# Optimization experiments

Measured on AMD Instinct MI355X. Metric: run time of the kernel, lower is better.

## Reference

```python
import jax, jax.numpy as jnp
import numpy as np

B, S, D, H = 2, 2048, 1024, 16
DK = D // H
NEG = -1.0e9


def setup_inputs() -> dict:
    key = jax.random.key(0)
    ks = jax.random.split(key, 12)
    scale = 1.0 / np.sqrt(D)
    return {
        "Q": jax.random.normal(ks[0], (B, S, D), jnp.float32),
        "K": jax.random.normal(ks[1], (B, S, D), jnp.float32),
        "V": jax.random.normal(ks[2], (B, S, D), jnp.float32),
        "Wq": jax.random.normal(ks[3], (D, D), jnp.float32) * scale,
        "bq": jnp.zeros((D,), jnp.float32),
        "Wk": jax.random.normal(ks[4], (D, D), jnp.float32) * scale,
        "bk": jnp.zeros((D,), jnp.float32),
        "Wv": jax.random.normal(ks[5], (D, D), jnp.float32) * scale,
        "bv": jnp.zeros((D,), jnp.float32),
        "Wo": jax.random.normal(ks[6], (D, D), jnp.float32) * scale,
        "bo": jnp.zeros((D,), jnp.float32),
        "src_mask": jnp.ones((B, S), jnp.int32),
    }


def reference(Q, K, V, Wq, bq, Wk, bk, Wv, bv, Wo, bo, src_mask):
    # Dropout layers are identity in eval mode.
    def heads(x, W, b):
        y = x @ W + b                      # [B,S,D]
        return y.reshape(B, S, H, DK).transpose(0, 2, 1, 3)  # [B,H,S,DK]

    q = heads(Q, Wq, bq)
    k = heads(K, Wk, bk)
    v = heads(V, Wv, bv)

    scores = jnp.einsum("bhqd,bhkd->bhqk", q, k) / np.sqrt(DK)  # [B,H,S,S]
    mask = src_mask[:, None, None, :]  # [B,1,1,S] broadcasts over heads/queries
    scores = jnp.where(mask == 0, NEG, scores)
    attn = jax.nn.softmax(scores, axis=-1)
    out = jnp.einsum("bhqk,bhkd->bhqd", attn, v)  # [B,H,S,DK]
    out = out.transpose(0, 2, 1, 3).reshape(B, S, D)
    return out @ Wo + bo
```

## Files before the change

kernel.cpp:

```cpp
#include <hip/hip_runtime.h>
#include <hip/hip_bf16.h>
#include <cstdint>

#define B_ 2
#define S_ 2048
#define D_ 1024
#define H_ 16
#define DK_ 64

typedef __bf16 bf16x8 __attribute__((ext_vector_type(8)));
typedef float f32x4 __attribute__((ext_vector_type(4)));
typedef unsigned int u32x4 __attribute__((ext_vector_type(4)));

typedef __attribute__((address_space(3))) void lds_void_t;
typedef const __attribute__((address_space(1))) void gbl_void_t;

__device__ __forceinline__ unsigned short f2bf(float x) {
    unsigned int u = __builtin_bit_cast(unsigned int, x);
    u += 0x7fffu + ((u >> 16) & 1u);
    return (unsigned short)(u >> 16);
}

__device__ __forceinline__ float exp2fast(float x) {
    float r;
    asm("v_exp_f32 %0, %1" : "=v"(r) : "v"(x));
    return r;
}

__device__ __forceinline__ unsigned cvtpk(float a, float b) {
    unsigned r;
    asm("v_cvt_pk_bf16_f32 %0, %1, %2" : "=v"(r) : "v"(a), "v"(b));
    return r;
}

__device__ __forceinline__ void gload16(const void* g, void* lds) {
    __builtin_amdgcn_global_load_lds((gbl_void_t*)(uintptr_t)g,
                                     (lds_void_t*)(unsigned)(uintptr_t)lds,
                                     16, 0, 0);
}

__device__ __forceinline__ bf16x8 lds_read8(const unsigned short* p) {
    return __builtin_bit_cast(bf16x8, *(const u32x4*)p);
}

__device__ __forceinline__ f32x4 mfma16(bf16x8 a, bf16x8 b, f32x4 c) {
    return __builtin_amdgcn_mfma_f32_16x16x32_bf16(a, b, c, 0, 0, 0);
}

__global__ void cast3_kernel(const float* __restrict__ Q, const float* __restrict__ K,
                             const float* __restrict__ V, unsigned short* __restrict__ Qc,
                             unsigned short* __restrict__ Kc, unsigned short* __restrict__ Vc,
                             int n4) {
    const int z = blockIdx.z;
    const float* in = (z == 0) ? Q : (z == 1) ? K : V;
    unsigned short* out = (z == 0) ? Qc : (z == 1) ? Kc : Vc;
    int i = blockIdx.x * 256 + threadIdx.x;
    if (i >= n4) return;
    const float4 v = reinterpret_cast<const float4*>(in)[i];
    unsigned long long pk = (unsigned long long)f2bf(v.x)
                          | ((unsigned long long)f2bf(v.y) << 16)
                          | ((unsigned long long)f2bf(v.z) << 32)
                          | ((unsigned long long)f2bf(v.w) << 48);
    reinterpret_cast<unsigned long long*>(out)[i] = pk;
}

__global__ void transpose4_kernel(const float* __restrict__ Wq, const float* __restrict__ Wk,
                                  const float* __restrict__ Wv, const float* __restrict__ Wo,
                                  unsigned short* __restrict__ WqT, unsigned short* __restrict__ WkT,
                                  unsigned short* __restrict__ WvT, unsigned short* __restrict__ WoT) {
    const int z = blockIdx.z;
    const float* W = (z == 0) ? Wq : (z == 1) ? Wk : (z == 2) ? Wv : Wo;
    unsigned short* Wt = (z == 0) ? WqT : (z == 1) ? WkT : (z == 2) ? WvT : WoT;
    __shared__ float t[32][33];
    const int bx = blockIdx.x, by = blockIdx.y;
    const int tx = threadIdx.x & 31, ty = threadIdx.x >> 5;
#pragma unroll
    for (int j = 0; j < 4; j++)
        t[ty + 8 * j][tx] = W[(size_t)(by * 32 + ty + 8 * j) * D_ + bx * 32 + tx];
    __syncthreads();
#pragma unroll
    for (int j = 0; j < 4; j++)
        Wt[(size_t)(bx * 32 + ty + 8 * j) * D_ + by * 32 + tx] = f2bf(t[tx][ty + 8 * j]);
}

__global__ __launch_bounds__(256, 3) void qkv_gemm(
    const unsigned short* __restrict__ Qc, const unsigned short* __restrict__ Kc,
    const unsigned short* __restrict__ Vc, const unsigned short* __restrict__ WqT,
    const unsigned short* __restrict__ WkT, const unsigned short* __restrict__ WvT,
    const float* __restrict__ bq, const float* __restrict__ bk,
    const float* __restrict__ bvv, unsigned short* __restrict__ qb,
    unsigned short* __restrict__ kb, unsigned short* __restrict__ vTb, float qs) {
    constexpr int Kd = 1024;
    __shared__ __align__(16) unsigned short As[128 * 32];
    __shared__ __align__(16) unsigned short Bs[128 * 32];
    __shared__ __align__(16) unsigned short Cs[128 * 136];
    const int z = blockIdx.z;
    const unsigned short* A  = (z == 0) ? Qc : (z == 1) ? Kc : Vc;
    const unsigned short* Bt = (z == 0) ? WqT : (z == 1) ? WkT : WvT;
    const float* bias = (z == 0) ? bq : (z == 1) ? bk : bvv;
    const float cscale = (z == 0) ? qs : 1.0f;

    const int tid = threadIdx.x;
    const int l = tid & 63, w = tid >> 6;
    const int lr = l & 15, g = l >> 4;
    const int wr = w & 1, wc = w >> 1;
    const int m0 = blockIdx.y * 128, n0 = blockIdx.x * 128;

    f32x4 acc[4][4] = {};

    const int mr = tid >> 2;
    const int kk = (tid & 3) * 8;
    const unsigned short* a_src = A + (size_t)(m0 + mr) * Kd + kk;
    const unsigned short* b_src = Bt + (size_t)(n0 + mr) * Kd + kk;
    char* asb = (char*)As + w * 1024;
    char* bsb = (char*)Bs + w * 1024;

    for (int k0 = 0; k0 < Kd; k0 += 32) {
        __syncthreads();
        gload16(a_src + k0,           asb);
        gload16(a_src + 64 * Kd + k0, asb + 4096);
        gload16(b_src + k0,           bsb);
        gload16(b_src + 64 * Kd + k0, bsb + 4096);
        __syncthreads();
        bf16x8 av[4], bv[4];
#pragma unroll
        for (int mi = 0; mi < 4; mi++)
            av[mi] = lds_read8(&As[(wr * 64 + mi * 16 + lr) * 32 + g * 8]);
#pragma unroll
        for (int ni = 0; ni < 4; ni++)
            bv[ni] = lds_read8(&Bs[(wc * 64 + ni * 16 + lr) * 32 + g * 8]);
#pragma unroll
        for (int mi = 0; mi < 4; mi++)
#pragma unroll
            for (int ni = 0; ni < 4; ni++)
                acc[mi][ni] = mfma16(av[mi], bv[ni], acc[mi][ni]);
    }

    if (z == 2) {
#pragma unroll
        for (int ni = 0; ni < 4; ni++) {
            const int cl = wc * 64 + ni * 16 + lr;
            const float bcol = bias[n0 + cl];
#pragma unroll
            for (int mi = 0; mi < 4; mi++) {
                const int rw = wr * 64 + mi * 16 + 4 * g;
                uint2 pk;
                pk.x = cvtpk(acc[mi][ni][0] + bcol, acc[mi][ni][1] + bcol);
                pk.y = cvtpk(acc[mi][ni][2] + bcol, acc[mi][ni][3] + bcol);
                *reinterpret_cast<uint2*>(&Cs[cl * 136 + rw]) = pk;
            }
        }
        __syncthreads();
        const int s0g = m0 & 2047;
        const int bb  = m0 >> 11;
#pragma unroll
        for (int it = 0; it < 8; ++it) {
            const int cl = it * 16 + (tid >> 4);
            const int sc = tid & 15;
            const int cg = n0 + cl;
            const int hh = cg >> 6, dk = cg & 63;
            const u32x4 vv = *reinterpret_cast<const u32x4*>(&Cs[cl * 136 + sc * 8]);
            *reinterpret_cast<u32x4*>(
                &vTb[(((size_t)(bb * H_ + hh) * DK_ + dk) << 11) + s0g + sc * 8]) = vv;
        }
    } else {
#pragma unroll
        for (int ni = 0; ni < 4; ni++) {
            const int col = n0 + wc * 64 + ni * 16 + lr;
            const float bcol = bias[col];
#pragma unroll
            for (int mi = 0; mi < 4; mi++) {
#pragma unroll
                for (int r = 0; r < 4; r++) {
                    const int row = m0 + wr * 64 + mi * 16 + 4 * g + r;
                    const float v = (acc[mi][ni][r] + bcol) * cscale;
                    const int b = row >> 11, s = row & 2047, h = col >> 6, dk = col & 63;
                    unsigned short* out = z ? kb : qb;
                    out[(((size_t)(b * H_ + h) * S_ + s) << 6) + dk] = f2bf(v);
                }
            }
        }
    }
}

__global__ __launch_bounds__(256, 2) void gemm_out(
    const unsigned short* __restrict__ A, const unsigned short* __restrict__ Bt,
    const float* __restrict__ bias, float* __restrict__ C) {
    constexpr int Kd = 1024;
    __shared__ __align__(16) unsigned short As[128 * 32];
    __shared__ __align__(16) unsigned short Bs[128 * 32];
    const int tid = threadIdx.x;
    const int l = tid & 63, w = tid >> 6;
    const int lr = l & 15, g = l >> 4;
    const int wr = w & 1, wc = w >> 1;
    const int m0 = blockIdx.y * 128, n0 = blockIdx.x * 128;

    f32x4 acc[4][4] = {};
    const int mr = tid >> 2;
    const int kk = (tid & 3) * 8;
    const unsigned short* a_src = A + (size_t)(m0 + mr) * Kd + kk;
    const unsigned short* b_src = Bt + (size_t)(n0 + mr) * Kd + kk;
    char* asb = (char*)As + w * 1024;
    char* bsb = (char*)Bs + w * 1024;

    for (int k0 = 0; k0 < Kd; k0 += 32) {
        __syncthreads();
        gload16(a_src + k0,           asb);
        gload16(a_src + 64 * Kd + k0, asb + 4096);
        gload16(b_src + k0,           bsb);
        gload16(b_src + 64 * Kd + k0, bsb + 4096);
        __syncthreads();
        bf16x8 av[4], bv[4];
#pragma unroll
        for (int mi = 0; mi < 4; mi++)
            av[mi] = lds_read8(&As[(wr * 64 + mi * 16 + lr) * 32 + g * 8]);
#pragma unroll
        for (int ni = 0; ni < 4; ni++)
            bv[ni] = lds_read8(&Bs[(wc * 64 + ni * 16 + lr) * 32 + g * 8]);
#pragma unroll
        for (int mi = 0; mi < 4; mi++)
#pragma unroll
            for (int ni = 0; ni < 4; ni++)
                acc[mi][ni] = mfma16(av[mi], bv[ni], acc[mi][ni]);
    }

#pragma unroll
    for (int ni = 0; ni < 4; ni++) {
        const int col = n0 + wc * 64 + ni * 16 + lr;
        const float bcol = bias[col];
#pragma unroll
        for (int mi = 0; mi < 4; mi++)
#pragma unroll
            for (int r = 0; r < 4; r++) {
                const int row = m0 + wr * 64 + mi * 16 + 4 * g + r;
                C[(size_t)row * D_ + col] = acc[mi][ni][r] + bcol;
            }
    }
}

__global__ __launch_bounds__(512, 4) void attn64(
    const unsigned short* __restrict__ q, const unsigned short* __restrict__ kmat,
    const unsigned short* __restrict__ vT, const int* __restrict__ mask,
    unsigned short* __restrict__ aout) {
    __shared__ __align__(16) unsigned short k_lds[2][64 * 64];
    __shared__ __align__(16) unsigned short v_lds[2][64 * 64];
    __shared__ __align__(16) unsigned short p_lds[8][16 * 72];
    __shared__ int mflag;

    const int tid = threadIdx.x;
    const int l = tid & 63, w = tid >> 6;
    const int lr = l & 15, g = l >> 4;
    const int bh = blockIdx.y;
    const int b = bh >> 4, h = bh & 15;
    const int q0 = blockIdx.x * 128;

    const size_t base = (size_t)bh * S_ * DK_;
    const size_t vbase = (size_t)bh * DK_ * S_;
    const float FM = 14.0f;

    bf16x8 qf[2];
#pragma unroll
    for (int ks = 0; ks < 2; ks++)
        qf[ks] = __builtin_bit_cast(bf16x8,
            *(const u32x4*)(q + base + (size_t)(q0 + w * 16 + lr) * 64 + ks * 32 + g * 8));

    const u32x4 ones_u = {0x3F803F80u, 0x3F803F80u, 0x3F803F80u, 0x3F803F80u};
    const bf16x8 ones = __builtin_bit_cast(bf16x8, ones_u);

    f32x4 O[4] = {};
    f32x4 lrun = {};
    unsigned short* pw = &p_lds[w][0];

    const int srow = tid >> 3;
    const int ssl  = (tid & 7) ^ (srow & 7);
    const unsigned short* ksrc = kmat + base + (size_t)srow * DK_ + ssl * 8;
    const unsigned short* vsrc = vT + vbase + (size_t)srow * S_ + ssl * 8;
    const int* mrow = mask + b * S_;

    if (tid == 0) mflag = 0;
    gload16(ksrc, (char*)&k_lds[0][0] + w * 1024);
    gload16(vsrc, (char*)&v_lds[0][0] + w * 1024);
    int ok = 1;
#pragma unroll
    for (int i = 0; i < 4; i++) ok &= (mrow[tid + i * 512] != 0);
    __syncthreads();
    if (!__all(ok)) mflag = 1;
    __syncthreads();
    const int maskany = mflag;

    auto body = [&](int t, const unsigned short* kc, const unsigned short* vc,
                    char* kn, char* vn, bool pf) {
        const int kv0 = t * 64;
        if (pf) {
            gload16(ksrc + (size_t)(kv0 + 64) * DK_, kn + w * 1024);
            gload16(vsrc + (kv0 + 64),               vn + w * 1024);
        }

        f32x4 sacc[4];
#pragma unroll
        for (int n = 0; n < 4; n++) {
            const int row = n * 16 + lr;
            const int x = lr & 7;
            bf16x8 kf0 = lds_read8(&kc[row * 64 + (g ^ x) * 8]);
            bf16x8 kf1 = lds_read8(&kc[row * 64 + ((4 + g) ^ x) * 8]);
            f32x4 s = {};
            s = mfma16(kf0, qf[0], s);
            s = mfma16(kf1, qf[1], s);
            sacc[n] = s;
        }

        if (maskany) {
#pragma unroll
            for (int n = 0; n < 4; n++) {
                const int4 mm = *reinterpret_cast<const int4*>(&mrow[kv0 + n * 16 + 4 * g]);
                sacc[n][0] = mm.x ? sacc[n][0] : -3.0e8f;
                sacc[n][1] = mm.y ? sacc[n][1] : -3.0e8f;
                sacc[n][2] = mm.z ? sacc[n][2] : -3.0e8f;
                sacc[n][3] = mm.w ? sacc[n][3] : -3.0e8f;
            }
        }

#pragma unroll
        for (int n = 0; n < 4; n++) {
            const float e0 = exp2fast(sacc[n][0] - FM);
            const float e1 = exp2fast(sacc[n][1] - FM);
            const float e2 = exp2fast(sacc[n][2] - FM);
            const float e3 = exp2fast(sacc[n][3] - FM);
            uint2 pk;
            pk.x = cvtpk(e0, e1);
            pk.y = cvtpk(e2, e3);
            *reinterpret_cast<uint2*>(&pw[lr * 72 + n * 16 + 4 * g]) = pk;
        }

        f32x4 osum = {};
#pragma unroll
        for (int k2 = 0; k2 < 2; k2++) {
            bf16x8 pa = lds_read8(&pw[lr * 72 + k2 * 32 + 8 * g]);
            osum = mfma16(pa, ones, osum);
#pragma unroll
            for (int n = 0; n < 4; n++) {
                const int row = n * 16 + lr;
                const int ph = (k2 * 4 + g) ^ (lr & 7);
                bf16x8 bvf = lds_read8(&vc[row * 64 + ph * 8]);
                O[n] = mfma16(pa, bvf, O[n]);
            }
        }
        lrun += osum;

        __syncthreads();
    };

    for (int t = 0; t < S_ / 64; t += 2) {
        body(t,     &k_lds[0][0], &v_lds[0][0], (char*)&k_lds[1][0], (char*)&v_lds[1][0],
             true);
        body(t + 1, &k_lds[1][0], &v_lds[1][0], (char*)&k_lds[0][0], (char*)&v_lds[0][0],
             t + 2 < S_ / 64);
    }

#pragma unroll
    for (int r = 0; r < 4; r++) {
        const float inv = 1.0f / lrun[r];
        const int srw = q0 + w * 16 + 4 * g + r;
#pragma unroll
        for (int n = 0; n < 4; n++) {
            const int col = h * 64 + n * 16 + lr;
            aout[(size_t)(b * S_ + srw) * D_ + col] = f2bf(O[n][r] * inv);
        }
    }
}

extern "C" void kernel_launch(void* const* d_in, const int* in_sizes, int n_in,
                              void* d_out, int out_size, void* d_ws, size_t ws_size,
                              hipStream_t stream) {
    const float* Q  = (const float*)d_in[0];
    const float* K  = (const float*)d_in[1];
    const float* V  = (const float*)d_in[2];
    const float* Wq = (const float*)d_in[3];
    const float* bq = (const float*)d_in[4];
    const float* Wk = (const float*)d_in[5];
    const float* bk = (const float*)d_in[6];
    const float* Wv = (const float*)d_in[7];
    const float* bv = (const float*)d_in[8];
    const float* Wo = (const float*)d_in[9];
    const float* bo = (const float*)d_in[10];
    const int*   mk = (const int*)d_in[11];

    char* ws = (char*)d_ws;
    unsigned short* Qc  = (unsigned short*)(ws + (0ull  << 20));
    unsigned short* Kc  = (unsigned short*)(ws + (8ull  << 20));
    unsigned short* Vc  = (unsigned short*)(ws + (16ull << 20));
    unsigned short* WqT = (unsigned short*)(ws + (24ull << 20));
    unsigned short* WkT = (unsigned short*)(ws + (26ull << 20));
    unsigned short* WvT = (unsigned short*)(ws + (28ull << 20));
    unsigned short* WoT = (unsigned short*)(ws + (30ull << 20));
    unsigned short* qb  = (unsigned short*)(ws + (32ull << 20));
    unsigned short* kb  = (unsigned short*)(ws + (40ull << 20));
    unsigned short* vTb = (unsigned short*)(ws + (48ull << 20));
    unsigned short* ab  = (unsigned short*)(ws + (56ull << 20));

    const int n4 = (B_ * S_ * D_) / 4;
    dim3 cg(n4 / 256, 1, 3);
    cast3_kernel<<<cg, 256, 0, stream>>>(Q, K, V, Qc, Kc, Vc, n4);
    dim3 tg(32, 32, 4);
    transpose4_kernel<<<tg, 256, 0, stream>>>(Wq, Wk, Wv, Wo, WqT, WkT, WvT, WoT);

    const float qs = 0.125f * 1.44269504088896340736f;
    dim3 gq(8, 32, 3);
    qkv_gemm<<<gq, 256, 0, stream>>>(Qc, Kc, Vc, WqT, WkT, WvT,
                                     bq, bk, bv, qb, kb, vTb, qs);

    dim3 ag(16, 32);
    attn64<<<ag, 512, 0, stream>>>(qb, kb, vTb, mk, ab);

    dim3 gg(8, 32);
    gemm_out<<<gg, 256, 0, stream>>>(ab, WoT, bo, (float*)d_out);
}
```

Measured before the change: 129.6 us.

## Merge cast and weight-transpose kernels, raise gemm_out occupancy, prioritize attention MFMA

Combines the activation cast and the four weight transposes into a single launch, where z<3 casts Q/K/V and z==3 transposes the weights, saving one kernel launch and its gap. The grid for z==3 is n4/256 = 4096 blocks, which exactly covers 4 weights × 1024 tiles. It also raises gemm_out's launch-bounds occupancy hint from 2 to 3 and wraps the attention MFMA sections in s_setprio so those waves are favoured over others while issuing matrix ops. The occupancy hint may force register spills, and the priority hints may have little effect.

After: 126.5 us. 2.4% less time.

```diff
diff --git a/kernel.cpp b/kernel.cpp
--- a/kernel.cpp
+++ b/kernel.cpp
@@ -47,40 +47,41 @@
     return __builtin_amdgcn_mfma_f32_16x16x32_bf16(a, b, c, 0, 0, 0);
 }
 
-__global__ void cast3_kernel(const float* __restrict__ Q, const float* __restrict__ K,
-                             const float* __restrict__ V, unsigned short* __restrict__ Qc,
-                             unsigned short* __restrict__ Kc, unsigned short* __restrict__ Vc,
-                             int n4) {
+__global__ void prep_kernel(const float* __restrict__ Q, const float* __restrict__ K,
+                            const float* __restrict__ V, const float* __restrict__ Wq,
+                            const float* __restrict__ Wk, const float* __restrict__ Wv,
+                            const float* __restrict__ Wo, unsigned short* __restrict__ Qc,
+                            unsigned short* __restrict__ Kc, unsigned short* __restrict__ Vc,
+                            unsigned short* __restrict__ WqT, unsigned short* __restrict__ WkT,
+                            unsigned short* __restrict__ WvT, unsigned short* __restrict__ WoT) {
     const int z = blockIdx.z;
-    const float* in = (z == 0) ? Q : (z == 1) ? K : V;
-    unsigned short* out = (z == 0) ? Qc : (z == 1) ? Kc : Vc;
-    int i = blockIdx.x * 256 + threadIdx.x;
-    if (i >= n4) return;
-    const float4 v = reinterpret_cast<const float4*>(in)[i];
-    unsigned long long pk = (unsigned long long)f2bf(v.x)
-                          | ((unsigned long long)f2bf(v.y) << 16)
-                          | ((unsigned long long)f2bf(v.z) << 32)
-                          | ((unsigned long long)f2bf(v.w) << 48);
-    reinterpret_cast<unsigned long long*>(out)[i] = pk;
-}
-
-__global__ void transpose4_kernel(const float* __restrict__ Wq, const float* __restrict__ Wk,
-                                  const float* __restrict__ Wv, const float* __restrict__ Wo,
-                                  unsigned short* __restrict__ WqT, unsigned short* __restrict__ WkT,
-                                  unsigned short* __restrict__ WvT, unsigned short* __restrict__ WoT) {
-    const int z = blockIdx.z;
-    const float* W = (z == 0) ? Wq : (z == 1) ? Wk : (z == 2) ? Wv : Wo;
-    unsigned short* Wt = (z == 0) ? WqT : (z == 1) ? WkT : (z == 2) ? WvT : WoT;
     __shared__ float t[32][33];
-    const int bx = blockIdx.x, by = blockIdx.y;
-    const int tx = threadIdx.x & 31, ty = threadIdx.x >> 5;
-#pragma unroll
-    for (int j = 0; j < 4; j++)
-        t[ty + 8 * j][tx] = W[(size_t)(by * 32 + ty + 8 * j) * D_ + bx * 32 + tx];
-    __syncthreads();
-#pragma unroll
-    for (int j = 0; j < 4; j++)
-        Wt[(size_t)(bx * 32 + ty + 8 * j) * D_ + by * 32 + tx] = f2bf(t[tx][ty + 8 * j]);
+    if (z < 3) {
+        const float* in = (z == 0) ? Q : (z == 1) ? K : V;
+        unsigned short* out = (z == 0) ? Qc : (z == 1) ? Kc : Vc;
+        const int i = blockIdx.x * 256 + threadIdx.x;
+        const float4 v = reinterpret_cast<const float4*>(in)[i];
+        unsigned long long pk = (unsigned long long)f2bf(v.x)
+                              | ((unsigned long long)f2bf(v.y) << 16)
+                              | ((unsigned long long)f2bf(v.z) << 32)
+                              | ((unsigned long long)f2bf(v.w) << 48);
+        reinterpret_cast<unsigned long long*>(out)[i] = pk;
+    } else {
+        const int wsel = blockIdx.x >> 10;
+        const int rem  = blockIdx.x & 1023;
+        const int bx = rem & 31, by = rem >> 5;
+        const float* W = (wsel == 0) ? Wq : (wsel == 1) ? Wk : (wsel == 2) ? Wv : Wo;
+        unsigned short* Wt = (wsel == 0) ? WqT : (wsel == 1) ? WkT
+                            : (wsel == 2) ? WvT : WoT;
+        const int tx = threadIdx.x & 31, ty = threadIdx.x >> 5;
+#pragma unroll
+        for (int j = 0; j < 4; j++)
+            t[ty + 8 * j][tx] = W[(size_t)(by * 32 + ty + 8 * j) * D_ + bx * 32 + tx];
+        __syncthreads();
+#pragma unroll
+        for (int j = 0; j < 4; j++)
+            Wt[(size_t)(bx * 32 + ty + 8 * j) * D_ + by * 32 + tx] = f2bf(t[tx][ty + 8 * j]);
+    }
 }
 
 __global__ __launch_bounds__(256, 3) void qkv_gemm(
@@ -183,7 +184,7 @@
     }
 }
 
-__global__ __launch_bounds__(256, 2) void gemm_out(
+__global__ __launch_bounds__(256, 3) void gemm_out(
     const unsigned short* __restrict__ A, const unsigned short* __restrict__ Bt,
     const float* __restrict__ bias, float* __restrict__ C) {
     constexpr int Kd = 1024;
@@ -297,6 +298,7 @@
         }
 
         f32x4 sacc[4];
+        __builtin_amdgcn_s_setprio(1);
 #pragma unroll
         for (int n = 0; n < 4; n++) {
             const int row = n * 16 + lr;
@@ -308,6 +310,7 @@
             s = mfma16(kf1, qf[1], s);
             sacc[n] = s;
         }
+        __builtin_amdgcn_s_setprio(0);
 
         if (maskany) {
 #pragma unroll
@@ -333,6 +336,7 @@
         }
 
         f32x4 osum = {};
+        __builtin_amdgcn_s_setprio(1);
 #pragma unroll
         for (int k2 = 0; k2 < 2; k2++) {
             bf16x8 pa = lds_read8(&pw[lr * 72 + k2 * 32 + 8 * g]);
@@ -345,6 +349,7 @@
                 O[n] = mfma16(pa, bvf, O[n]);
             }
         }
+        __builtin_amdgcn_s_setprio(0);
         lrun += osum;
 
         __syncthreads();
@@ -399,10 +404,9 @@
     unsigned short* ab  = (unsigned short*)(ws + (56ull << 20));
 
     const int n4 = (B_ * S_ * D_) / 4;
-    dim3 cg(n4 / 256, 1, 3);
-    cast3_kernel<<<cg, 256, 0, stream>>>(Q, K, V, Qc, Kc, Vc, n4);
-    dim3 tg(32, 32, 4);
-    transpose4_kernel<<<tg, 256, 0, stream>>>(Wq, Wk, Wv, Wo, WqT, WkT, WvT, WoT);
+    dim3 pg(n4 / 256, 1, 4);
+    prep_kernel<<<pg, 256, 0, stream>>>(Q, K, V, Wq, Wk, Wv, Wo,
+                                        Qc, Kc, Vc, WqT, WkT, WvT, WoT);
 
     const float qs = 0.125f * 1.44269504088896340736f;
     dim3 gq(8, 32, 3);
```
